# Kernel optimization log

Hardware: AMD Instinct MI355X
Metric: run time of the kernel (lower is better)

Reference implementation:

```python
import jax, jax.numpy as jnp
import numpy as np

H = 128
IN = 5
EPS = 1e-5


def lstm(x, Wih, Whh, bih, bhh):
    # x: [B,T,D]; PyTorch gate order i,f,g,o along 4H axis
    B, T, _ = x.shape
    xW = jnp.einsum('btd,gd->btg', x, Wih) + bih + bhh  # [B,T,4H]
    WhhT = Whh.T

    def step(carry, xt):
        h, c = carry
        g = xt + h @ WhhT
        i, f, gg, o = jnp.split(g, 4, axis=-1)
        i = jax.nn.sigmoid(i)
        f = jax.nn.sigmoid(f)
        gg = jnp.tanh(gg)
        o = jax.nn.sigmoid(o)
        c = f * c + i * gg
        h = o * jnp.tanh(c)
        return (h, c), h

    h0 = jnp.zeros((B, H), x.dtype)
    _, hs = jax.lax.scan(step, (h0, h0), jnp.swapaxes(xW, 0, 1))
    return jnp.swapaxes(hs, 0, 1)  # [B,T,H]


def batchnorm(x, gamma, beta):
    # training-mode BN over (batch, time) per channel; x: [B,T,H]
    mean = jnp.mean(x, axis=(0, 1))
    var = jnp.var(x, axis=(0, 1))
    return (x - mean) * (gamma * jax.lax.rsqrt(var + EPS)) + beta


def forward_one(x, Wih1, Whh1, bih1, bhh1, g1, b1, Wih2, Whh2, bih2, bhh2, g2, b2, fcW, fcb):
    out = lstm(x, Wih1, Whh1, bih1, bhh1)
    out = batchnorm(out, g1, b1)
    # dropout is identity (eval / deterministic reference)
    out = lstm(out, Wih2, Whh2, bih2, bhh2)
    out = batchnorm(out, g2, b2)
    emb = out[:, -1, :] @ fcW.T + fcb  # [B,128]
    norm = jnp.sqrt(jnp.sum(emb * emb, axis=1, keepdims=True))
    return emb / jnp.maximum(norm, 1e-12)  # F.normalize p=2


def setup_inputs() -> dict:
    key = jax.random.key(0)
    ks = jax.random.split(key, 20)
    B, T = 512, 128
    s_in = 1.0 / np.sqrt(H)
    d = {
        'a': jax.random.normal(ks[0], (B, T, IN), jnp.float32),
        'p': jax.random.normal(ks[1], (B, T, IN), jnp.float32),
        'n': jax.random.normal(ks[2], (B, T, IN), jnp.float32),
        'Wih1': jax.random.uniform(ks[3], (4 * H, IN), jnp.float32, -s_in, s_in),
        'Whh1': jax.random.uniform(ks[4], (4 * H, H), jnp.float32, -s_in, s_in),
        'bih1': jax.random.uniform(ks[5], (4 * H,), jnp.float32, -s_in, s_in),
        'bhh1': jax.random.uniform(ks[6], (4 * H,), jnp.float32, -s_in, s_in),
        'g1': jnp.ones((H,), jnp.float32),
        'b1': jnp.zeros((H,), jnp.float32),
        'Wih2': jax.random.uniform(ks[7], (4 * H, H), jnp.float32, -s_in, s_in),
        'Whh2': jax.random.uniform(ks[8], (4 * H, H), jnp.float32, -s_in, s_in),
        'bih2': jax.random.uniform(ks[9], (4 * H,), jnp.float32, -s_in, s_in),
        'bhh2': jax.random.uniform(ks[10], (4 * H,), jnp.float32, -s_in, s_in),
        'g2': jnp.ones((H,), jnp.float32),
        'b2': jnp.zeros((H,), jnp.float32),
        'fcW': jax.random.uniform(ks[11], (H, H), jnp.float32, -s_in, s_in),
        'fcb': jax.random.uniform(ks[12], (H,), jnp.float32, -s_in, s_in),
    }
    return d


def reference(a, p, n, Wih1, Whh1, bih1, bhh1, g1, b1, Wih2, Whh2, bih2, bhh2, g2, b2, fcW, fcb):
    f = lambda x: forward_one(x, Wih1, Whh1, bih1, bhh1, g1, b1, Wih2, Whh2, bih2, bhh2, g2, b2, fcW, fcb)
    return (f(a), f(p), f(n))
```

## Files before the change

kernel.cpp:

```cpp
#include <hip/hip_runtime.h>


typedef __attribute__((ext_vector_type(8))) _Float16 half8;
typedef __attribute__((ext_vector_type(4))) float f32x4;

#define TS 128
#define HID 128
#define NGATE 512
#define INQ 5
#define INV_N (1.0f/65536.0f)

#define BAR() asm volatile("s_waitcnt lgkmcnt(0)\n\ts_barrier" ::: "memory")

__device__ __forceinline__ float rcpf(float x) { return __builtin_amdgcn_rcpf(x); }
__device__ __forceinline__ float clamp20(float x) { return fminf(fmaxf(x, -20.0f), 20.0f); }

__global__ void prep_whhT(const float* __restrict__ Whh1,
                          const float* __restrict__ Whh2,
                          _Float16* __restrict__ whhT1,
                          _Float16* __restrict__ whhT2) {
  int i = blockIdx.x * 256 + threadIdx.x;
  int which = i >> 16, idx = i & 65535;
  int k = idx >> 9, g = idx & 511;
  const float* src = which ? Whh2 : Whh1;
  _Float16* dst = which ? whhT2 : whhT1;
  dst[idx] = (_Float16)src[g * HID + k];
}

__global__ void prep_bias(const float* __restrict__ bih1, const float* __restrict__ bhh1,
                          const float* __restrict__ bih2, const float* __restrict__ bhh2,
                          float* __restrict__ b1c, float* __restrict__ b2c) {
  int i = blockIdx.x * 256 + threadIdx.x;
  if (i < 512) b1c[i] = bih1[i] + bhh1[i];
  else         b2c[i - 512] = bih2[i - 512] + bhh2[i - 512];
}

__device__ __forceinline__ _Float16 lstm_cell(float zi, float zf, float zg, float zo,
                                              float& c) {
  zg = clamp20(zg);
  float ei = __expf(-zi);
  float eg = __expf(-2.0f * zg);
  float ef = __expf(-zf);
  float fv = rcpf(1.0f + ef);
  float ig = (1.0f - eg) * rcpf((1.0f + ei) * (1.0f + eg));
  float cc = fv * c + ig;
  c = cc;
  float ccl = clamp20(cc);
  float eo = __expf(-zo);
  float ec = __expf(-2.0f * ccl);
  float hv = (1.0f - ec) * rcpf((1.0f + eo) * (1.0f + ec));
  return (_Float16)hv;
}

__global__ __launch_bounds__(512, 2) void lstm1_kernel(
    const float* __restrict__ xa, const float* __restrict__ xp, const float* __restrict__ xn,
    const float* __restrict__ Wih1,
    const float* __restrict__ b1c,
    const _Float16* __restrict__ whhT,
    _Float16* __restrict__ hs1,
    float* __restrict__ s1sum, float* __restrict__ s1sq) {
  const int wg = blockIdx.x;
  const int inp = wg >> 5;
  const int rloc = (wg & 31) * 16;
  const float* x = (inp == 0) ? xa : ((inp == 1) ? xp : xn);

  const int tid = threadIdx.x;
  const int w = tid >> 6;
  const int lane = tid & 63;
  const int l15 = lane & 15;
  const int quad = lane >> 4;
  const int col = w * 16 + l15;
  const int kb = quad * 8;

  __shared__ _Float16 hbuf[2][16][136];
  __shared__ _Float16 xt_lds[TS][16][8];

  for (int i = tid; i < 16 * 136; i += 512) ((_Float16*)hbuf[0])[i] = (_Float16)0.0f;
  for (int i = tid; i < TS * 16 * 8; i += 512) ((_Float16*)xt_lds)[i] = (_Float16)0.0f;
  __syncthreads();
  for (int i = tid; i < 16 * TS * INQ; i += 512) {
    int r = i / 640, rem = i - r * 640;
    int t = rem / 5, d = rem - t * 5;
    xt_lds[t][r][d] = (_Float16)x[(rloc + r) * 640 + rem];
  }

  half8 bh[4][4];
#pragma unroll
  for (int kt = 0; kt < 4; ++kt)
#pragma unroll
    for (int gt = 0; gt < 4; ++gt) {
      int gcol = gt * 128 + col;
      half8 v;
#pragma unroll
      for (int j = 0; j < 8; ++j) v[j] = whhT[(kt * 32 + kb + j) * NGATE + gcol];
      bh[kt][gt] = v;
    }
  half8 bx[4];
#pragma unroll
  for (int gt = 0; gt < 4; ++gt) {
    half8 v = {0, 0, 0, 0, 0, 0, 0, 0};
    if (quad == 0) {
#pragma unroll
      for (int j = 0; j < 5; ++j) v[j] = (_Float16)Wih1[(gt * 128 + col) * INQ + j];
    }
    bx[gt] = v;
  }
  f32x4 biasv[4];
#pragma unroll
  for (int gt = 0; gt < 4; ++gt) {
    float b = b1c[gt * 128 + col];
    biasv[gt][0] = b; biasv[gt][1] = b; biasv[gt][2] = b; biasv[gt][3] = b;
  }

  float c[4] = {0, 0, 0, 0};
  float ssum = 0.0f, ssq = 0.0f;
  _Float16* hs1w = hs1 + (size_t)wg * TS * 16 * HID;

  __syncthreads();

  for (int t = 0; t < TS; ++t) {
    half8 ax = {0, 0, 0, 0, 0, 0, 0, 0};
    if (quad == 0) ax = *(const half8*)&xt_lds[t][l15][0];
    f32x4 acc[4];
#pragma unroll
    for (int gt = 0; gt < 4; ++gt)
      acc[gt] = __builtin_amdgcn_mfma_f32_16x16x32_f16(ax, bx[gt], biasv[gt], 0, 0, 0);
    BAR();
    half8 ah[4];
#pragma unroll
    for (int kt = 0; kt < 4; ++kt)
      ah[kt] = *(const half8*)&hbuf[t & 1][l15][kt * 32 + kb];
#pragma unroll
    for (int kt = 0; kt < 4; ++kt)
#pragma unroll
      for (int gt = 0; gt < 4; ++gt)
        acc[gt] = __builtin_amdgcn_mfma_f32_16x16x32_f16(ah[kt], bh[kt][gt], acc[gt], 0, 0, 0);
#pragma unroll
    for (int r = 0; r < 4; ++r) {
      _Float16 hh = lstm_cell(acc[0][r], acc[1][r], acc[2][r], acc[3][r], c[r]);
      float hr = (float)hh;
      ssum += hr; ssq += hr * hr;
      int row = quad * 4 + r;
      hbuf[(t + 1) & 1][row][col] = hh;
      hs1w[((size_t)t * 16 + row) * HID + col] = hh;
    }
  }
  float s = ssum, q = ssq;
  s += __shfl_xor(s, 16); s += __shfl_xor(s, 32);
  q += __shfl_xor(q, 16); q += __shfl_xor(q, 32);
  if (quad == 0) {
    atomicAdd(&s1sum[inp * HID + col], s);
    atomicAdd(&s1sq[inp * HID + col], q);
  }
}

__global__ void finalize1_kernel(const float* __restrict__ s1sum, const float* __restrict__ s1sq,
                                 const float* __restrict__ g1, const float* __restrict__ b1,
                                 float* __restrict__ scale1, float* __restrict__ shift1) {
  int i = blockIdx.x * 128 + threadIdx.x;
  int h = i & 127;
  float m = s1sum[i] * INV_N;
  float v = s1sq[i] * INV_N - m * m;
  float s = g1[h] * rsqrtf(v + 1e-5f);
  scale1[i] = s;
  shift1[i] = b1[h] - m * s;
}

__global__ void w2s_kernel(const float* __restrict__ scale1, const float* __restrict__ Wih2,
                           _Float16* __restrict__ w2s) {
  int i = blockIdx.x * 256 + threadIdx.x;
  int inp = i >> 16, rem = i & 65535, k = rem >> 9, g = rem & 511;
  w2s[i] = (_Float16)(scale1[inp * HID + k] * Wih2[g * HID + k]);
}

__global__ void bias2_kernel(const float* __restrict__ shift1, const float* __restrict__ Wih2,
                             const float* __restrict__ b2c, float* __restrict__ bias2eff) {
  int i = blockIdx.x * 512 + threadIdx.x;
  int inp = i >> 9, g = i & 511;
  float acc = b2c[g];
  for (int h = 0; h < HID; ++h) acc += shift1[inp * HID + h] * Wih2[g * HID + h];
  bias2eff[i] = acc;
}

__global__ __launch_bounds__(512, 2) void lstm2_kernel(
    const _Float16* __restrict__ hs1,
    const _Float16* __restrict__ whhT2,
    const _Float16* __restrict__ w2s,
    const float* __restrict__ bias2eff,
    _Float16* __restrict__ h_last,
    float* __restrict__ s2sum, float* __restrict__ s2sq) {
  const int wg = blockIdx.x;
  const int inp = wg >> 5;
  const int gr0 = wg * 16;

  const int tid = threadIdx.x;
  const int w = tid >> 6;
  const int lane = tid & 63;
  const int l15 = lane & 15;
  const int quad = lane >> 4;
  const int col = w * 16 + l15;
  const int kb = quad * 8;

  __shared__ _Float16 hbuf[2][16][136];
  for (int i = tid; i < 16 * 136; i += 512) ((_Float16*)hbuf[0])[i] = (_Float16)0.0f;

  const _Float16* w2sI = w2s + (size_t)inp * HID * NGATE;
  half8 bh[4][4], bxw[4][4];
#pragma unroll
  for (int kt = 0; kt < 4; ++kt)
#pragma unroll
    for (int gt = 0; gt < 4; ++gt) {
      int gcol = gt * 128 + col;
      half8 vh, vx;
#pragma unroll
      for (int j = 0; j < 8; ++j) {
        vh[j] = whhT2[(kt * 32 + kb + j) * NGATE + gcol];
        vx[j] = w2sI[(kt * 32 + kb + j) * NGATE + gcol];
      }
      bh[kt][gt] = vh;
      bxw[kt][gt] = vx;
    }
  f32x4 biasv[4];
#pragma unroll
  for (int gt = 0; gt < 4; ++gt) {
    float b = bias2eff[inp * NGATE + gt * 128 + col];
    biasv[gt][0] = b; biasv[gt][1] = b; biasv[gt][2] = b; biasv[gt][3] = b;
  }

  const _Float16* hg = hs1 + (size_t)wg * TS * 16 * HID;
  half8 a2A[4], a2B[4];
#pragma unroll
  for (int kt = 0; kt < 4; ++kt) {
    a2A[kt] = *(const half8*)&hg[(size_t)l15 * HID + kt * 32 + kb];
    a2B[kt] = *(const half8*)&hg[((size_t)1 * 16 + l15) * HID + kt * 32 + kb];
  }

  float c[4] = {0, 0, 0, 0};
  float ssum = 0.0f, ssq = 0.0f;

  __syncthreads();

  auto step = [&](int t, half8 (&cur)[4]) {
    f32x4 acc[4];
#pragma unroll
    for (int gt = 0; gt < 4; ++gt)
      acc[gt] = __builtin_amdgcn_mfma_f32_16x16x32_f16(cur[0], bxw[0][gt], biasv[gt], 0, 0, 0);
#pragma unroll
    for (int kt = 1; kt < 4; ++kt)
#pragma unroll
      for (int gt = 0; gt < 4; ++gt)
        acc[gt] = __builtin_amdgcn_mfma_f32_16x16x32_f16(cur[kt], bxw[kt][gt], acc[gt], 0, 0, 0);
    if (t + 2 < TS) {
#pragma unroll
      for (int kt = 0; kt < 4; ++kt)
        cur[kt] = *(const half8*)&hg[((size_t)(t + 2) * 16 + l15) * HID + kt * 32 + kb];
    }
    BAR();
    half8 ah[4];
#pragma unroll
    for (int kt = 0; kt < 4; ++kt)
      ah[kt] = *(const half8*)&hbuf[t & 1][l15][kt * 32 + kb];
#pragma unroll
    for (int kt = 0; kt < 4; ++kt)
#pragma unroll
      for (int gt = 0; gt < 4; ++gt)
        acc[gt] = __builtin_amdgcn_mfma_f32_16x16x32_f16(ah[kt], bh[kt][gt], acc[gt], 0, 0, 0);
#pragma unroll
    for (int r = 0; r < 4; ++r) {
      _Float16 hh = lstm_cell(acc[0][r], acc[1][r], acc[2][r], acc[3][r], c[r]);
      float hr = (float)hh;
      ssum += hr; ssq += hr * hr;
      int row = quad * 4 + r;
      hbuf[(t + 1) & 1][row][col] = hh;
      if (t == TS - 1) h_last[(gr0 + row) * HID + col] = hh;
    }
  };

  for (int t = 0; t < TS; t += 2) {
    step(t, a2A);
    step(t + 1, a2B);
  }

  float s = ssum, q = ssq;
  s += __shfl_xor(s, 16); s += __shfl_xor(s, 32);
  q += __shfl_xor(q, 16); q += __shfl_xor(q, 32);
  if (quad == 0) {
    atomicAdd(&s2sum[inp * HID + col], s);
    atomicAdd(&s2sq[inp * HID + col], q);
  }
}

__global__ __launch_bounds__(256, 1) void head_kernel(
    const _Float16* __restrict__ h_last,
    const float* __restrict__ s2sum, const float* __restrict__ s2sq,
    const float* __restrict__ g2, const float* __restrict__ b2,
    const float* __restrict__ fcW, const float* __restrict__ fcb,
    float* __restrict__ out) {
  const int wg = blockIdx.x;
  const int inp = wg >> 5;
  const int gr0 = wg * 16;
  const int tid = threadIdx.x;

  __shared__ float fcwT[128][132];
  __shared__ float bnh[16][132];
  __shared__ float s2[128], sh2[128];
  __shared__ float part[16][16];
  __shared__ float inv[16];

  if (tid < 128) {
    float m = s2sum[inp * HID + tid] * INV_N;
    float v = s2sq[inp * HID + tid] * INV_N - m * m;
    float s = g2[tid] * rsqrtf(v + 1e-5f);
    s2[tid] = s; sh2[tid] = b2[tid] - m * s;
  }
  for (int i = tid; i < 16384; i += 256) {
    int j = i >> 7, h = i & 127;
    fcwT[h][j] = fcW[i];
  }
  __syncthreads();
  {
    int row = tid >> 4, c0 = (tid & 15) * 8;
#pragma unroll
    for (int k = 0; k < 8; ++k) {
      int h = c0 + k;
      bnh[row][h] = (float)h_last[(gr0 + row) * HID + h] * s2[h] + sh2[h];
    }
  }
  __syncthreads();
  const int row = tid >> 4, jl = tid & 15;
  float emb[8];
  float sq = 0.0f;
#pragma unroll
  for (int jj = 0; jj < 8; ++jj) {
    int j = jl + jj * 16;
    float acc = fcb[j];
    for (int h = 0; h < HID; ++h) acc += bnh[row][h] * fcwT[h][j];
    emb[jj] = acc; sq += acc * acc;
  }
  part[row][jl] = sq;
  __syncthreads();
  if (tid < 16) {
    float s = 0.0f;
    for (int k = 0; k < 16; ++k) s += part[tid][k];
    float nrm = sqrtf(s);
    inv[tid] = 1.0f / fmaxf(nrm, 1e-12f);
  }
  __syncthreads();
#pragma unroll
  for (int jj = 0; jj < 8; ++jj)
    out[(gr0 + row) * HID + jl + jj * 16] = emb[jj] * inv[row];
}

extern "C" void kernel_launch(void* const* d_in, const int* in_sizes, int n_in,
                              void* d_out, int out_size, void* d_ws, size_t ws_size,
                              hipStream_t stream) {
  const float* a    = (const float*)d_in[0];
  const float* p    = (const float*)d_in[1];
  const float* nn   = (const float*)d_in[2];
  const float* Wih1 = (const float*)d_in[3];
  const float* Whh1 = (const float*)d_in[4];
  const float* bih1 = (const float*)d_in[5];
  const float* bhh1 = (const float*)d_in[6];
  const float* g1   = (const float*)d_in[7];
  const float* b1   = (const float*)d_in[8];
  const float* Wih2 = (const float*)d_in[9];
  const float* Whh2 = (const float*)d_in[10];
  const float* bih2 = (const float*)d_in[11];
  const float* bhh2 = (const float*)d_in[12];
  const float* g2   = (const float*)d_in[13];
  const float* b2   = (const float*)d_in[14];
  const float* fcW  = (const float*)d_in[15];
  const float* fcb  = (const float*)d_in[16];

  char* ws = (char*)d_ws;
  float* s1sum = (float*)(ws + 0);
  float* s1sq  = s1sum + 384;
  float* s2sum = s1sum + 768;
  float* s2sq  = s1sum + 1152;
  float* b1c   = (float*)(ws + 6144);
  float* b2c   = b1c + 512;
  float* scale1 = (float*)(ws + 10240);
  float* shift1 = scale1 + 384;
  float* bias2eff = (float*)(ws + 13312);
  _Float16* whhT1 = (_Float16*)(ws + 19456);
  _Float16* whhT2 = (_Float16*)(ws + 150528);
  _Float16* w2s   = (_Float16*)(ws + 281600);
  _Float16* hlast = (_Float16*)(ws + 674816);
  _Float16* hs1   = (_Float16*)(ws + 1068032);

  hipMemsetAsync(ws, 0, 6144, stream);

  prep_whhT<<<512, 256, 0, stream>>>(Whh1, Whh2, whhT1, whhT2);
  prep_bias<<<4, 256, 0, stream>>>(bih1, bhh1, bih2, bhh2, b1c, b2c);
  lstm1_kernel<<<96, 512, 0, stream>>>(a, p, nn, Wih1, b1c, whhT1, hs1, s1sum, s1sq);
  finalize1_kernel<<<3, 128, 0, stream>>>(s1sum, s1sq, g1, b1, scale1, shift1);
  w2s_kernel<<<768, 256, 0, stream>>>(scale1, Wih2, w2s);
  bias2_kernel<<<3, 512, 0, stream>>>(shift1, Wih2, b2c, bias2eff);
  lstm2_kernel<<<96, 512, 0, stream>>>(hs1, whhT2, w2s, bias2eff, hlast, s2sum, s2sq);
  head_kernel<<<96, 256, 0, stream>>>(hlast, s2sum, s2sq, g2, b2, fcW, fcb, (float*)d_out);
}
```

Before: 392.6 us.

## Process two 16-row tiles per workgroup in LSTM kernels with swizzled h layout

Each LSTM workgroup now runs two independent 16-row batch tiles (A and B), so the MFMA chains of the two tiles interleave and hide latency along the serial time recurrence. The grid shrinks from 96 to 48 workgroups. The hidden state in LDS uses a swizzled fragment-major layout so loads are contiguous, and hs1 is written in that layout via coalesced copies from LDS. Input x is pre-padded to fp16 in a separate prep kernel instead of staged per workgroup. The trade-off is fewer workgroups and more registers per workgroup, in exchange for more instruction-level parallelism per barrier.

New measurement: 605.9 us. +54.3%, slower.

```diff
diff --git a/kernel.cpp b/kernel.cpp
--- a/kernel.cpp
+++ b/kernel.cpp
@@ -7,33 +7,12 @@
 #define TS 128
 #define HID 128
 #define NGATE 512
-#define INQ 5
 #define INV_N (1.0f/65536.0f)
 
 #define BAR() asm volatile("s_waitcnt lgkmcnt(0)\n\ts_barrier" ::: "memory")
 
 __device__ __forceinline__ float rcpf(float x) { return __builtin_amdgcn_rcpf(x); }
 __device__ __forceinline__ float clamp20(float x) { return fminf(fmaxf(x, -20.0f), 20.0f); }
-
-__global__ void prep_whhT(const float* __restrict__ Whh1,
-                          const float* __restrict__ Whh2,
-                          _Float16* __restrict__ whhT1,
-                          _Float16* __restrict__ whhT2) {
-  int i = blockIdx.x * 256 + threadIdx.x;
-  int which = i >> 16, idx = i & 65535;
-  int k = idx >> 9, g = idx & 511;
-  const float* src = which ? Whh2 : Whh1;
-  _Float16* dst = which ? whhT2 : whhT1;
-  dst[idx] = (_Float16)src[g * HID + k];
-}
-
-__global__ void prep_bias(const float* __restrict__ bih1, const float* __restrict__ bhh1,
-                          const float* __restrict__ bih2, const float* __restrict__ bhh2,
-                          float* __restrict__ b1c, float* __restrict__ b2c) {
-  int i = blockIdx.x * 256 + threadIdx.x;
-  if (i < 512) b1c[i] = bih1[i] + bhh1[i];
-  else         b2c[i - 512] = bih2[i - 512] + bhh2[i - 512];
-}
 
 __device__ __forceinline__ _Float16 lstm_cell(float zi, float zf, float zg, float zo,
                                               float& c) {
@@ -52,17 +31,46 @@
   return (_Float16)hv;
 }
 
+__global__ void prep_whhT(const float* __restrict__ Whh1,
+                          const float* __restrict__ Whh2,
+                          _Float16* __restrict__ whhT1,
+                          _Float16* __restrict__ whhT2) {
+  int i = blockIdx.x * 256 + threadIdx.x;
+  int which = i >> 16, idx = i & 65535;
+  int k = idx >> 9, g = idx & 511;
+  const float* src = which ? Whh2 : Whh1;
+  _Float16* dst = which ? whhT2 : whhT1;
+  dst[idx] = (_Float16)src[g * HID + k];
+}
+
+__global__ void prep_bias(const float* __restrict__ bih1, const float* __restrict__ bhh1,
+                          const float* __restrict__ bih2, const float* __restrict__ bhh2,
+                          float* __restrict__ b1c, float* __restrict__ b2c) {
+  int i = blockIdx.x * 256 + threadIdx.x;
+  if (i < 512) b1c[i] = bih1[i] + bhh1[i];
+  else         b2c[i - 512] = bih2[i - 512] + bhh2[i - 512];
+}
+
+__global__ void prep_xpad(const float* __restrict__ xa, const float* __restrict__ xp,
+                          const float* __restrict__ xn, _Float16* __restrict__ xpad) {
+  int i = blockIdx.x * 256 + threadIdx.x;
+  int tile = i >> 14, rem = i & 16383;
+  int t = rem >> 7, r = (rem >> 3) & 15, d = i & 7;
+  int inp = tile >> 5, rloc = (tile & 31) * 16;
+  const float* x = (inp == 0) ? xa : ((inp == 1) ? xp : xn);
+  xpad[i] = (d < 5) ? (_Float16)x[(rloc + r) * 640 + t * 5 + d] : (_Float16)0.0f;
+}
+
 __global__ __launch_bounds__(512, 2) void lstm1_kernel(
-    const float* __restrict__ xa, const float* __restrict__ xp, const float* __restrict__ xn,
+    const _Float16* __restrict__ xpad,
     const float* __restrict__ Wih1,
     const float* __restrict__ b1c,
     const _Float16* __restrict__ whhT,
     _Float16* __restrict__ hs1,
     float* __restrict__ s1sum, float* __restrict__ s1sq) {
   const int wg = blockIdx.x;
-  const int inp = wg >> 5;
-  const int rloc = (wg & 31) * 16;
-  const float* x = (inp == 0) ? xa : ((inp == 1) ? xp : xn);
+  const int tA = wg * 2, tB = tA + 1;
+  const int inp = tA >> 5;
 
   const int tid = threadIdx.x;
   const int w = tid >> 6;
@@ -72,17 +80,12 @@
   const int col = w * 16 + l15;
   const int kb = quad * 8;
 
-  __shared__ _Float16 hbuf[2][16][136];
-  __shared__ _Float16 xt_lds[TS][16][8];
-
-  for (int i = tid; i < 16 * 136; i += 512) ((_Float16*)hbuf[0])[i] = (_Float16)0.0f;
-  for (int i = tid; i < TS * 16 * 8; i += 512) ((_Float16*)xt_lds)[i] = (_Float16)0.0f;
-  __syncthreads();
-  for (int i = tid; i < 16 * TS * INQ; i += 512) {
-    int r = i / 640, rem = i - r * 640;
-    int t = rem / 5, d = rem - t * 5;
-    xt_lds[t][r][d] = (_Float16)x[(rloc + r) * 640 + rem];
-  }
+  __shared__ _Float16 hb[2][2][2048];
+
+  for (int i = tid; i < 2 * 2 * 2048; i += 512) ((_Float16*)hb)[i] = (_Float16)0.0f;
+
+  const int rbase = (quad * 16 + l15) * 8;
+  const int wslot = (w >> 1) * 512 + (((w & 1) * 2 + (l15 >> 3)) * 16 + quad * 4) * 8 + (l15 & 7);
 
   half8 bh[4][4];
 #pragma unroll
@@ -101,7 +104,7 @@
     half8 v = {0, 0, 0, 0, 0, 0, 0, 0};
     if (quad == 0) {
 #pragma unroll
-      for (int j = 0; j < 5; ++j) v[j] = (_Float16)Wih1[(gt * 128 + col) * INQ + j];
+      for (int j = 0; j < 5; ++j) v[j] = (_Float16)Wih1[(gt * 128 + col) * 5 + j];
     }
     bx[gt] = v;
   }
@@ -112,38 +115,66 @@
     biasv[gt][0] = b; biasv[gt][1] = b; biasv[gt][2] = b; biasv[gt][3] = b;
   }
 
-  float c[4] = {0, 0, 0, 0};
+  half8 xpA = {0,0,0,0,0,0,0,0}, xpB = {0,0,0,0,0,0,0,0};
+  if (quad == 0) {
+    xpA = *(const half8*)&xpad[((size_t)(tA * TS + 0) * 16 + l15) * 8];
+    xpB = *(const half8*)&xpad[((size_t)(tB * TS + 0) * 16 + l15) * 8];
+  }
+
+  float cA[4] = {0,0,0,0}, cB[4] = {0,0,0,0};
   float ssum = 0.0f, ssq = 0.0f;
-  _Float16* hs1w = hs1 + (size_t)wg * TS * 16 * HID;
 
   __syncthreads();
 
   for (int t = 0; t < TS; ++t) {
-    half8 ax = {0, 0, 0, 0, 0, 0, 0, 0};
-    if (quad == 0) ax = *(const half8*)&xt_lds[t][l15][0];
-    f32x4 acc[4];
+    f32x4 aA[4], aB[4];
 #pragma unroll
     for (int gt = 0; gt < 4; ++gt)
-      acc[gt] = __builtin_amdgcn_mfma_f32_16x16x32_f16(ax, bx[gt], biasv[gt], 0, 0, 0);
+      aA[gt] = __builtin_amdgcn_mfma_f32_16x16x32_f16(xpA, bx[gt], biasv[gt], 0, 0, 0);
+#pragma unroll
+    for (int gt = 0; gt < 4; ++gt)
+      aB[gt] = __builtin_amdgcn_mfma_f32_16x16x32_f16(xpB, bx[gt], biasv[gt], 0, 0, 0);
+    if (t + 1 < TS && quad == 0) {
+      xpA = *(const half8*)&xpad[((size_t)(tA * TS + t + 1) * 16 + l15) * 8];
+      xpB = *(const half8*)&xpad[((size_t)(tB * TS + t + 1) * 16 + l15) * 8];
+    }
     BAR();
-    half8 ah[4];
-#pragma unroll
-    for (int kt = 0; kt < 4; ++kt)
-      ah[kt] = *(const half8*)&hbuf[t & 1][l15][kt * 32 + kb];
-#pragma unroll
-    for (int kt = 0; kt < 4; ++kt)
-#pragma unroll
-      for (int gt = 0; gt < 4; ++gt)
-        acc[gt] = __builtin_amdgcn_mfma_f32_16x16x32_f16(ah[kt], bh[kt][gt], acc[gt], 0, 0, 0);
+    if (t > 0) {
+      float2 cpA = *(const float2*)&hb[0][t & 1][tid * 4];
+      float2 cpB = *(const float2*)&hb[1][t & 1][tid * 4];
+      *(float2*)&hs1[((size_t)tA * TS + (t - 1)) * 2048 + tid * 4] = cpA;
+      *(float2*)&hs1[((size_t)tB * TS + (t - 1)) * 2048 + tid * 4] = cpB;
+    }
+#pragma unroll
+    for (int kt = 0; kt < 4; ++kt) {
+      half8 ahA = *(const half8*)&hb[0][t & 1][kt * 512 + rbase];
+      half8 ahB = *(const half8*)&hb[1][t & 1][kt * 512 + rbase];
+#pragma unroll
+      for (int gt = 0; gt < 4; ++gt)
+        aA[gt] = __builtin_amdgcn_mfma_f32_16x16x32_f16(ahA, bh[kt][gt], aA[gt], 0, 0, 0);
+#pragma unroll
+      for (int gt = 0; gt < 4; ++gt)
+        aB[gt] = __builtin_amdgcn_mfma_f32_16x16x32_f16(ahB, bh[kt][gt], aB[gt], 0, 0, 0);
+    }
+    const int wb = (t + 1) & 1;
 #pragma unroll
     for (int r = 0; r < 4; ++r) {
-      _Float16 hh = lstm_cell(acc[0][r], acc[1][r], acc[2][r], acc[3][r], c[r]);
-      float hr = (float)hh;
-      ssum += hr; ssq += hr * hr;
-      int row = quad * 4 + r;
-      hbuf[(t + 1) & 1][row][col] = hh;
-      hs1w[((size_t)t * 16 + row) * HID + col] = hh;
-    }
+      _Float16 hhA = lstm_cell(aA[0][r], aA[1][r], aA[2][r], aA[3][r], cA[r]);
+      float hrA = (float)hhA;
+      ssum += hrA; ssq += hrA * hrA;
+      hb[0][wb][wslot + r * 8] = hhA;
+      _Float16 hhB = lstm_cell(aB[0][r], aB[1][r], aB[2][r], aB[3][r], cB[r]);
+      float hrB = (float)hhB;
+      ssum += hrB; ssq += hrB * hrB;
+      hb[1][wb][wslot + r * 8] = hhB;
+    }
+  }
+  BAR();
+  {
+    float2 cpA = *(const float2*)&hb[0][0][tid * 4];
+    float2 cpB = *(const float2*)&hb[1][0][tid * 4];
+    *(float2*)&hs1[((size_t)tA * TS + (TS - 1)) * 2048 + tid * 4] = cpA;
+    *(float2*)&hs1[((size_t)tB * TS + (TS - 1)) * 2048 + tid * 4] = cpB;
   }
   float s = ssum, q = ssq;
   s += __shfl_xor(s, 16); s += __shfl_xor(s, 32);
@@ -190,8 +221,9 @@
     _Float16* __restrict__ h_last,
     float* __restrict__ s2sum, float* __restrict__ s2sq) {
   const int wg = blockIdx.x;
-  const int inp = wg >> 5;
-  const int gr0 = wg * 16;
+  const int tA = wg * 2, tB = tA + 1;
+  const int inp = tA >> 5;
+  const int gr0A = tA * 16, gr0B = tB * 16;
 
   const int tid = threadIdx.x;
   const int w = tid >> 6;
@@ -201,8 +233,11 @@
   const int col = w * 16 + l15;
   const int kb = quad * 8;
 
-  __shared__ _Float16 hbuf[2][16][136];
-  for (int i = tid; i < 16 * 136; i += 512) ((_Float16*)hbuf[0])[i] = (_Float16)0.0f;
+  __shared__ _Float16 hb[2][2][2048];
+  for (int i = tid; i < 2 * 2 * 2048; i += 512) ((_Float16*)hb)[i] = (_Float16)0.0f;
+
+  const int rbase = (quad * 16 + l15) * 8;
+  const int wslot = (w >> 1) * 512 + (((w & 1) * 2 + (l15 >> 3)) * 16 + quad * 4) * 8 + (l15 & 7);
 
   const _Float16* w2sI = w2s + (size_t)inp * HID * NGATE;
   half8 bh[4][4], bxw[4][4];
@@ -227,58 +262,73 @@
     biasv[gt][0] = b; biasv[gt][1] = b; biasv[gt][2] = b; biasv[gt][3] = b;
   }
 
-  const _Float16* hg = hs1 + (size_t)wg * TS * 16 * HID;
-  half8 a2A[4], a2B[4];
+  const _Float16* hgA = hs1 + (size_t)tA * TS * 2048;
+  const _Float16* hgB = hs1 + (size_t)tB * TS * 2048;
+  half8 xpA[4], xpB[4];
 #pragma unroll
   for (int kt = 0; kt < 4; ++kt) {
-    a2A[kt] = *(const half8*)&hg[(size_t)l15 * HID + kt * 32 + kb];
-    a2B[kt] = *(const half8*)&hg[((size_t)1 * 16 + l15) * HID + kt * 32 + kb];
-  }
-
-  float c[4] = {0, 0, 0, 0};
+    xpA[kt] = *(const half8*)&hgA[kt * 512 + rbase];
+    xpB[kt] = *(const half8*)&hgB[kt * 512 + rbase];
+  }
+
+  float cA[4] = {0,0,0,0}, cB[4] = {0,0,0,0};
   float ssum = 0.0f, ssq = 0.0f;
 
   __syncthreads();
 
-  auto step = [&](int t, half8 (&cur)[4]) {
-    f32x4 acc[4];
+  for (int t = 0; t < TS; ++t) {
+    f32x4 aA[4], aB[4];
 #pragma unroll
     for (int gt = 0; gt < 4; ++gt)
-      acc[gt] = __builtin_amdgcn_mfma_f32_16x16x32_f16(cur[0], bxw[0][gt], biasv[gt], 0, 0, 0);
-#pragma unroll
-    for (int kt = 1; kt < 4; ++kt)
-#pragma unroll
-      for (int gt = 0; gt < 4; ++gt)
-        acc[gt] = __builtin_amdgcn_mfma_f32_16x16x32_f16(cur[kt], bxw[kt][gt], acc[gt], 0, 0, 0);
-    if (t + 2 < TS) {
-#pragma unroll
-      for (int kt = 0; kt < 4; ++kt)
-        cur[kt] = *(const half8*)&hg[((size_t)(t + 2) * 16 + l15) * HID + kt * 32 + kb];
+      aA[gt] = __builtin_amdgcn_mfma_f32_16x16x32_f16(xpA[0], bxw[0][gt], biasv[gt], 0, 0, 0);
+#pragma unroll
+    for (int gt = 0; gt < 4; ++gt)
+      aB[gt] = __builtin_amdgcn_mfma_f32_16x16x32_f16(xpB[0], bxw[0][gt], biasv[gt], 0, 0, 0);
+#pragma unroll
+    for (int kt = 1; kt < 4; ++kt) {
+#pragma unroll
+      for (int gt = 0; gt < 4; ++gt)
+        aA[gt] = __builtin_amdgcn_mfma_f32_16x16x32_f16(xpA[kt], bxw[kt][gt], aA[gt], 0, 0, 0);
+#pragma unroll
+      for (int gt = 0; gt < 4; ++gt)
+        aB[gt] = __builtin_amdgcn_mfma_f32_16x16x32_f16(xpB[kt], bxw[kt][gt], aB[gt], 0, 0, 0);
+    }
+    if (t + 1 < TS) {
+#pragma unroll
+      for (int kt = 0; kt < 4; ++kt) {
+        xpA[kt] = *(const half8*)&hgA[(size_t)(t + 1) * 2048 + kt * 512 + rbase];
+        xpB[kt] = *(const half8*)&hgB[(size_t)(t + 1) * 2048 + kt * 512 + rbase];
+      }
     }
     BAR();
-    half8 ah[4];
-#pragma unroll
-    for (int kt = 0; kt < 4; ++kt)
-      ah[kt] = *(const half8*)&hbuf[t & 1][l15][kt * 32 + kb];
-#pragma unroll
-    for (int kt = 0; kt < 4; ++kt)
-#pragma unroll
-      for (int gt = 0; gt < 4; ++gt)
-        acc[gt] = __builtin_amdgcn_mfma_f32_16x16x32_f16(ah[kt], bh[kt][gt], acc[gt], 0, 0, 0);
+#pragma unroll
+    for (int kt = 0; kt < 4; ++kt) {
+      half8 ahA = *(const half8*)&hb[0][t & 1][kt * 512 + rbase];
+      half8 ahB = *(const half8*)&hb[1][t & 1][kt * 512 + rbase];
+#pragma unroll
+      for (int gt = 0; gt < 4; ++gt)
+        aA[gt] = __builtin_amdgcn_mfma_f32_16x16x32_f16(ahA, bh[kt][gt], aA[gt], 0, 0, 0);
+#pragma unroll
+      for (int gt = 0; gt < 4; ++gt)
+        aB[gt] = __builtin_amdgcn_mfma_f32_16x16x32_f16(ahB, bh[kt][gt], aB[gt], 0, 0, 0);
+    }
+    const int wb = (t + 1) & 1;
 #pragma unroll
     for (int r = 0; r < 4; ++r) {
-      _Float16 hh = lstm_cell(acc[0][r], acc[1][r], acc[2][r], acc[3][r], c[r]);
-      float hr = (float)hh;
-      ssum += hr; ssq += hr * hr;
-      int row = quad * 4 + r;
-      hbuf[(t + 1) & 1][row][col] = hh;
-      if (t == TS - 1) h_last[(gr0 + row) * HID + col] = hh;
-    }
-  };
-
-  for (int t = 0; t < TS; t += 2) {
-    step(t, a2A);
-    step(t + 1, a2B);
+      _Float16 hhA = lstm_cell(aA[0][r], aA[1][r], aA[2][r], aA[3][r], cA[r]);
+      float hrA = (float)hhA;
+      ssum += hrA; ssq += hrA * hrA;
+      hb[0][wb][wslot + r * 8] = hhA;
+      _Float16 hhB = lstm_cell(aB[0][r], aB[1][r], aB[2][r], aB[3][r], cB[r]);
+      float hrB = (float)hhB;
+      ssum += hrB; ssq += hrB * hrB;
+      hb[1][wb][wslot + r * 8] = hhB;
+      if (t == TS - 1) {
+        int row = quad * 4 + r;
+        h_last[(size_t)(gr0A + row) * HID + col] = hhA;
+        h_last[(size_t)(gr0B + row) * HID + col] = hhB;
+      }
+    }
   }
 
   float s = ssum, q = ssq;
@@ -386,16 +436,18 @@
   _Float16* whhT2 = (_Float16*)(ws + 150528);
   _Float16* w2s   = (_Float16*)(ws + 281600);
   _Float16* hlast = (_Float16*)(ws + 674816);
-  _Float16* hs1   = (_Float16*)(ws + 1068032);
+  _Float16* xpad  = (_Float16*)(ws + 1068032);
+  _Float16* hs1   = (_Float16*)(ws + 4213760);
 
   hipMemsetAsync(ws, 0, 6144, stream);
 
   prep_whhT<<<512, 256, 0, stream>>>(Whh1, Whh2, whhT1, whhT2);
   prep_bias<<<4, 256, 0, stream>>>(bih1, bhh1, bih2, bhh2, b1c, b2c);
-  lstm1_kernel<<<96, 512, 0, stream>>>(a, p, nn, Wih1, b1c, whhT1, hs1, s1sum, s1sq);
+  prep_xpad<<<6144, 256, 0, stream>>>(a, p, nn, xpad);
+  lstm1_kernel<<<48, 512, 0, stream>>>(xpad, Wih1, b1c, whhT1, hs1, s1sum, s1sq);
   finalize1_kernel<<<3, 128, 0, stream>>>(s1sum, s1sq, g1, b1, scale1, shift1);
   w2s_kernel<<<768, 256, 0, stream>>>(scale1, Wih2, w2s);
   bias2_kernel<<<3, 512, 0, stream>>>(shift1, Wih2, b2c, bias2eff);
-  lstm2_kernel<<<96, 512, 0, stream>>>(hs1, whhT2, w2s, bias2eff, hlast, s2sum, s2sq);
+  lstm2_kernel<<<48, 512, 0, stream>>>(hs1, whhT2, w2s, bias2eff, hlast, s2sum, s2sq);
   head_kernel<<<96, 256, 0, stream>>>(hlast, s2sum, s2sq, g2, b2, fcW, fcb, (float*)d_out);
 }
```
